# Performance work log

Hardware: AMD Instinct MI355X
Metric: run time of the kernel (lower is better)

Reference implementation:

```python
import jax, jax.numpy as jnp
import numpy as np

EPS = 1e-12  # torch F.normalize eps

def _normalize(x):
    n = jnp.linalg.norm(x, axis=-1, keepdims=True)
    return x / jnp.maximum(n, EPS)

def setup_inputs() -> dict:
    key = jax.random.key(0)
    k1, k2, k3, k4 = jax.random.split(key, 4)
    bs, P = 32, 256
    V = P * P                      # 65536 vertices
    F = 2 * (P - 1) ** 2           # 130050 faces
    C = 6                          # triangles per vertex ring
    points = jax.random.normal(k1, (bs, 3, V), dtype=jnp.float32)
    faces = jax.random.randint(k2, (F, 3), 0, V, dtype=jnp.int32)
    vert_tri_indices = jax.random.randint(k3, (V, C), 0, F, dtype=jnp.int32)
    vert_tri_weights = jax.random.uniform(k4, (V, C, 1), dtype=jnp.float32)
    return {"points": points, "faces": faces,
            "vert_tri_indices": vert_tri_indices,
            "vert_tri_weights": vert_tri_weights}

def reference(points, faces, vert_tri_indices, vert_tri_weights):
    # points: [bs, 3, V] -> vrt: [bs, V, 3]
    vrt = jnp.transpose(points, (0, 2, 1))
    # face normals: gather the 3 vertices of each face, cross, normalize
    v0 = vrt[:, faces[:, 0]]                       # [bs, F, 3]
    v1 = vrt[:, faces[:, 1]] - v0
    v2 = vrt[:, faces[:, 2]] - v0
    face_normals = _normalize(jnp.cross(v1, v2))   # [bs, F, 3]
    # vertex normals: weighted sum over each vertex's triangle ring
    fn_group = face_normals[:, vert_tri_indices]   # [bs, V, C, 3]
    vertex_normals = (fn_group * vert_tri_weights).sum(axis=-2)  # [bs, V, 3]
    return _normalize(vertex_normals)
```

## Files before the change

### kernel.cpp

```cpp
#include <hip/hip_runtime.h>
#include <hip/hip_bf16.h>


#define XCDS 8
#define BPX  4
#define FPT  2

typedef float f32x4 __attribute__((ext_vector_type(4)));

__device__ __forceinline__ float mulf_pin(float a, float b) {
  float t = a * b;
  asm("" : "+v"(t));
  return t;
}

__device__ __forceinline__ float3 cross_lhs(float ax, float ay, float az,
                                            float bx, float by, float bz) {
  float cx = __builtin_fmaf(ay, bz, -mulf_pin(az, by));
  float cy = __builtin_fmaf(az, bx, -mulf_pin(ax, bz));
  float cz = __builtin_fmaf(ax, by, -mulf_pin(ay, bx));
  return make_float3(cx, cy, cz);
}

__device__ __forceinline__ void nt_store_f4(float4* p, float x, float y,
                                            float z, float w) {
  f32x4 r;
  r[0] = x; r[1] = y; r[2] = z; r[3] = w;
  __builtin_nontemporal_store(r, (f32x4*)p);
}

__global__ __launch_bounds__(256) void rend13_pack(
    const float* __restrict__ points,
    float4*      __restrict__ ptsI,
    int V) {
  int xcd = blockIdx.x % XCDS;
  int g   = (blockIdx.x / XCDS) * 256 + threadIdx.x;
  int v   = g >> 2;
  int bl  = g & 3;
  int b   = xcd * BPX + bl;
  const float* pb = points + (size_t)b * 3 * V;
  float x = __builtin_nontemporal_load(pb + v);
  float y = __builtin_nontemporal_load(pb + V + v);
  float z = __builtin_nontemporal_load(pb + 2 * V + v);
  ptsI[((size_t)xcd * V + v) * BPX + bl] = make_float4(x, y, z, 0.0f);
}

__global__ __launch_bounds__(256) void rend13_face(
    const float4* __restrict__ ptsI,
    const int*    __restrict__ faces,
    float4*       __restrict__ fnI,
    int F, int V, int Q) {
  int xcd = blockIdx.x % XCDS;
  int g   = (blockIdx.x / XCDS) * 256 + threadIdx.x;
  int q   = g >> 2;
  int bl  = g & 3;
  if (q >= Q) return;

  int f0 = q;
  int f1 = q + Q;

  int a0 = __builtin_nontemporal_load(faces + 3 * f0 + 0);
  int a1 = __builtin_nontemporal_load(faces + 3 * f0 + 1);
  int a2 = __builtin_nontemporal_load(faces + 3 * f0 + 2);
  int b0 = __builtin_nontemporal_load(faces + 3 * f1 + 0);
  int b1 = __builtin_nontemporal_load(faces + 3 * f1 + 1);
  int b2 = __builtin_nontemporal_load(faces + 3 * f1 + 2);

  const float4* P = ptsI + (size_t)xcd * V * BPX;
  float4 pa0 = P[(size_t)a0 * BPX + bl];
  float4 pa1 = P[(size_t)a1 * BPX + bl];
  float4 pa2 = P[(size_t)a2 * BPX + bl];
  float4 pb0 = P[(size_t)b0 * BPX + bl];
  float4 pb1 = P[(size_t)b1 * BPX + bl];
  float4 pb2 = P[(size_t)b2 * BPX + bl];

  {
    float ax = pa1.x - pa0.x, ay = pa1.y - pa0.y, az = pa1.z - pa0.z;
    float bx = pa2.x - pa0.x, by = pa2.y - pa0.y, bz = pa2.z - pa0.z;
    float3 c = cross_lhs(ax, ay, az, bx, by, bz);
    float n = sqrtf((c.x * c.x + c.y * c.y) + c.z * c.z);
    float d = fmaxf(n, 1e-12f);
    nt_store_f4(fnI + ((size_t)xcd * F + f0) * BPX + bl,
                c.x / d, c.y / d, c.z / d, 0.0f);
  }
  {
    float ax = pb1.x - pb0.x, ay = pb1.y - pb0.y, az = pb1.z - pb0.z;
    float bx = pb2.x - pb0.x, by = pb2.y - pb0.y, bz = pb2.z - pb0.z;
    float3 c = cross_lhs(ax, ay, az, bx, by, bz);
    float n = sqrtf((c.x * c.x + c.y * c.y) + c.z * c.z);
    float d = fmaxf(n, 1e-12f);
    nt_store_f4(fnI + ((size_t)xcd * F + f1) * BPX + bl,
                c.x / d, c.y / d, c.z / d, 0.0f);
  }
}

__global__ __launch_bounds__(256) void rend13_vertex(
    const float4* __restrict__ fnI,
    const int*    __restrict__ vti,
    const float*  __restrict__ vtw,
    float*        __restrict__ out,
    int F, int V) {
  int xcd = blockIdx.x % XCDS;
  int g   = (blockIdx.x / XCDS) * 256 + threadIdx.x;
  int v   = g >> 2;
  int bl  = g & 3;
  if (v >= V) return;

  const int2*   t2 = (const int2*)(vti + (size_t)v * 6);
  const float2* w2 = (const float2*)(vtw + (size_t)v * 6);
  int2   t01 = t2[0], t23 = t2[1], t45 = t2[2];
  float2 w01 = w2[0], w23 = w2[1], w45 = w2[2];
  int   idx[6] = {t01.x, t01.y, t23.x, t23.y, t45.x, t45.y};
  float wgt[6] = {w01.x, w01.y, w23.x, w23.y, w45.x, w45.y};

  float sx = 0.f, sy = 0.f, sz = 0.f;
#pragma unroll
  for (int c = 0; c < 6; ++c) {
    float4 nr = fnI[((size_t)xcd * F + idx[c]) * BPX + bl];
    sx += nr.x * wgt[c];
    sy += nr.y * wgt[c];
    sz += nr.z * wgt[c];
  }

  float n = sqrtf((sx * sx + sy * sy) + sz * sz);
  float d = fmaxf(n, 1e-12f);

  int b = xcd * BPX + bl;
  size_t o = ((size_t)b * V + v) * 3;
  __builtin_nontemporal_store(sx / d, out + o + 0);
  __builtin_nontemporal_store(sy / d, out + o + 1);
  __builtin_nontemporal_store(sz / d, out + o + 2);
}

__global__ __launch_bounds__(256) void rend13_face_fb(
    const float* __restrict__ points,
    const int*   __restrict__ faces,
    float4*      __restrict__ fnorm,
    int F, int V) {
  int f = blockIdx.x * blockDim.x + threadIdx.x;
  int b = blockIdx.y;
  if (f >= F) return;

  int i0 = faces[3 * f + 0];
  int i1 = faces[3 * f + 1];
  int i2 = faces[3 * f + 2];

  const float* pb = points + (size_t)b * 3 * V;
  float ax = pb[i1] - pb[i0], ay = pb[V + i1] - pb[V + i0], az = pb[2 * V + i1] - pb[2 * V + i0];
  float bx = pb[i2] - pb[i0], by = pb[V + i2] - pb[V + i0], bz = pb[2 * V + i2] - pb[2 * V + i0];

  float3 c = cross_lhs(ax, ay, az, bx, by, bz);

  float n = sqrtf((c.x * c.x + c.y * c.y) + c.z * c.z);
  float d = fmaxf(n, 1e-12f);

  fnorm[(size_t)b * F + f] = make_float4(c.x / d, c.y / d, c.z / d, 0.0f);
}

__global__ __launch_bounds__(256) void rend13_vertex_fb(
    const float4* __restrict__ fnorm,
    const int*    __restrict__ vti,
    const float*  __restrict__ vtw,
    float*        __restrict__ out,
    int F, int V) {
  int v = blockIdx.x * blockDim.x + threadIdx.x;
  int b = blockIdx.y;
  if (v >= V) return;

  const float4* fb = fnorm + (size_t)b * F;
  float sx = 0.f, sy = 0.f, sz = 0.f;
#pragma unroll
  for (int c = 0; c < 6; ++c) {
    int    idx = vti[v * 6 + c];
    float  w   = vtw[v * 6 + c];
    float4 nr  = fb[idx];
    sx += nr.x * w;
    sy += nr.y * w;
    sz += nr.z * w;
  }
  float n = sqrtf((sx * sx + sy * sy) + sz * sz);
  float d = fmaxf(n, 1e-12f);
  size_t o = ((size_t)b * V + v) * 3;
  out[o + 0] = sx / d;
  out[o + 1] = sy / d;
  out[o + 2] = sz / d;
}

extern "C" void kernel_launch(void* const* d_in, const int* in_sizes, int n_in,
                              void* d_out, int out_size, void* d_ws, size_t ws_size,
                              hipStream_t stream) {
  const float* points = (const float*)d_in[0];
  const int*   faces  = (const int*)d_in[1];
  const int*   vti    = (const int*)d_in[2];
  const float* vtw    = (const float*)d_in[3];
  float*       out    = (float*)d_out;

  const int F  = in_sizes[1] / 3;
  const int V  = in_sizes[2] / 6;
  const int bs = (int)(in_sizes[0] / (3 * (size_t)V));

  const size_t ptsI_bytes = (size_t)bs * V * sizeof(float4);
  const size_t fnI_bytes  = (size_t)bs * F * sizeof(float4);

  const bool fast_ok = (ws_size >= ptsI_bytes + fnI_bytes) &&
                       (bs == XCDS * BPX) && (V % 256 == 0) && (F % FPT == 0);

  if (fast_ok) {
    float4* ptsI = (float4*)d_ws;
    float4* fnI  = (float4*)((char*)d_ws + ptsI_bytes);
    const int Q   = F / FPT;
    const int ppb = (V * BPX) / 256;
    const int fqb = (Q * 4 + 255) / 256;
    const int vqb = (V * BPX) / 256;

    rend13_pack<<<dim3(XCDS * ppb), dim3(256), 0, stream>>>(points, ptsI, V);
    rend13_face<<<dim3(XCDS * fqb), dim3(256), 0, stream>>>(ptsI, faces, fnI, F, V, Q);
    rend13_vertex<<<dim3(XCDS * vqb), dim3(256), 0, stream>>>(fnI, vti, vtw, out, F, V);
  } else if (ws_size >= fnI_bytes) {
    float4* fnorm = (float4*)d_ws;
    rend13_face_fb<<<dim3((F + 255) / 256, bs), dim3(256), 0, stream>>>(
        points, faces, fnorm, F, V);
    rend13_vertex_fb<<<dim3((V + 255) / 256, bs), dim3(256), 0, stream>>>(
        fnorm, vti, vtw, out, F, V);
  }
}
```

Measured before the change: 165.3 us.

## Pack intermediates as 12-byte float3 per batch lane, three faces per thread

Changes the interleaved point and face-normal workspaces from float4 per batch lane to a packed 3-float layout of 12 floats per vertex or face, which cuts intermediate memory traffic by a quarter. The face kernel now handles three faces per thread instead of two. The vertex kernel loads its indices and weights as scalar nontemporal loads. The cost is that gathers become unaligned scalar 3-float loads instead of single 16-byte vector loads, which may raise the instruction count and the number of memory transactions.

Measured after the change: 163.4 us. About the same (-1.2%).

```diff
diff --git a/kernel.cpp b/kernel.cpp
--- a/kernel.cpp
+++ b/kernel.cpp
@@ -4,9 +4,7 @@
 
 #define XCDS 8
 #define BPX  4
-#define FPT  2
-
-typedef float f32x4 __attribute__((ext_vector_type(4)));
+#define FPT  3
 
 __device__ __forceinline__ float mulf_pin(float a, float b) {
   float t = a * b;
@@ -22,16 +20,9 @@
   return make_float3(cx, cy, cz);
 }
 
-__device__ __forceinline__ void nt_store_f4(float4* p, float x, float y,
-                                            float z, float w) {
-  f32x4 r;
-  r[0] = x; r[1] = y; r[2] = z; r[3] = w;
-  __builtin_nontemporal_store(r, (f32x4*)p);
-}
-
-__global__ __launch_bounds__(256) void rend13_pack(
+__global__ __launch_bounds__(256) void rend16_pack(
     const float* __restrict__ points,
-    float4*      __restrict__ ptsI,
+    float*       __restrict__ ptsP,
     int V) {
   int xcd = blockIdx.x % XCDS;
   int g   = (blockIdx.x / XCDS) * 256 + threadIdx.x;
@@ -42,13 +33,14 @@
   float x = __builtin_nontemporal_load(pb + v);
   float y = __builtin_nontemporal_load(pb + V + v);
   float z = __builtin_nontemporal_load(pb + 2 * V + v);
-  ptsI[((size_t)xcd * V + v) * BPX + bl] = make_float4(x, y, z, 0.0f);
-}
-
-__global__ __launch_bounds__(256) void rend13_face(
-    const float4* __restrict__ ptsI,
-    const int*    __restrict__ faces,
-    float4*       __restrict__ fnI,
+  float* e = ptsP + ((size_t)xcd * V + v) * 12 + 3 * bl;
+  e[0] = x; e[1] = y; e[2] = z;
+}
+
+__global__ __launch_bounds__(256) void rend16_face(
+    const float* __restrict__ ptsP,
+    const int*   __restrict__ faces,
+    float*       __restrict__ fnP,
     int F, int V, int Q) {
   int xcd = blockIdx.x % XCDS;
   int g   = (blockIdx.x / XCDS) * 256 + threadIdx.x;
@@ -58,6 +50,7 @@
 
   int f0 = q;
   int f1 = q + Q;
+  int f2 = q + 2 * Q;
 
   int a0 = __builtin_nontemporal_load(faces + 3 * f0 + 0);
   int a1 = __builtin_nontemporal_load(faces + 3 * f0 + 1);
@@ -65,40 +58,72 @@
   int b0 = __builtin_nontemporal_load(faces + 3 * f1 + 0);
   int b1 = __builtin_nontemporal_load(faces + 3 * f1 + 1);
   int b2 = __builtin_nontemporal_load(faces + 3 * f1 + 2);
-
-  const float4* P = ptsI + (size_t)xcd * V * BPX;
-  float4 pa0 = P[(size_t)a0 * BPX + bl];
-  float4 pa1 = P[(size_t)a1 * BPX + bl];
-  float4 pa2 = P[(size_t)a2 * BPX + bl];
-  float4 pb0 = P[(size_t)b0 * BPX + bl];
-  float4 pb1 = P[(size_t)b1 * BPX + bl];
-  float4 pb2 = P[(size_t)b2 * BPX + bl];
-
+  int c0 = __builtin_nontemporal_load(faces + 3 * f2 + 0);
+  int c1 = __builtin_nontemporal_load(faces + 3 * f2 + 1);
+  int c2 = __builtin_nontemporal_load(faces + 3 * f2 + 2);
+
+  const float* P = ptsP + (size_t)xcd * V * 12 + 3 * bl;
+  const float* ea0 = P + (size_t)a0 * 12;
+  const float* ea1 = P + (size_t)a1 * 12;
+  const float* ea2 = P + (size_t)a2 * 12;
+  const float* eb0 = P + (size_t)b0 * 12;
+  const float* eb1 = P + (size_t)b1 * 12;
+  const float* eb2 = P + (size_t)b2 * 12;
+  const float* ec0 = P + (size_t)c0 * 12;
+  const float* ec1 = P + (size_t)c1 * 12;
+  const float* ec2 = P + (size_t)c2 * 12;
+
+  float a0x = ea0[0], a0y = ea0[1], a0z = ea0[2];
+  float a1x = ea1[0], a1y = ea1[1], a1z = ea1[2];
+  float a2x = ea2[0], a2y = ea2[1], a2z = ea2[2];
+  float b0x = eb0[0], b0y = eb0[1], b0z = eb0[2];
+  float b1x = eb1[0], b1y = eb1[1], b1z = eb1[2];
+  float b2x = eb2[0], b2y = eb2[1], b2z = eb2[2];
+  float c0x = ec0[0], c0y = ec0[1], c0z = ec0[2];
+  float c1x = ec1[0], c1y = ec1[1], c1z = ec1[2];
+  float c2x = ec2[0], c2y = ec2[1], c2z = ec2[2];
+
+  float* O = fnP + (size_t)xcd * F * 12 + 3 * bl;
   {
-    float ax = pa1.x - pa0.x, ay = pa1.y - pa0.y, az = pa1.z - pa0.z;
-    float bx = pa2.x - pa0.x, by = pa2.y - pa0.y, bz = pa2.z - pa0.z;
+    float ax = a1x - a0x, ay = a1y - a0y, az = a1z - a0z;
+    float bx = a2x - a0x, by = a2y - a0y, bz = a2z - a0z;
     float3 c = cross_lhs(ax, ay, az, bx, by, bz);
     float n = sqrtf((c.x * c.x + c.y * c.y) + c.z * c.z);
     float d = fmaxf(n, 1e-12f);
-    nt_store_f4(fnI + ((size_t)xcd * F + f0) * BPX + bl,
-                c.x / d, c.y / d, c.z / d, 0.0f);
+    float* o = O + (size_t)f0 * 12;
+    __builtin_nontemporal_store(c.x / d, o + 0);
+    __builtin_nontemporal_store(c.y / d, o + 1);
+    __builtin_nontemporal_store(c.z / d, o + 2);
   }
   {
-    float ax = pb1.x - pb0.x, ay = pb1.y - pb0.y, az = pb1.z - pb0.z;
-    float bx = pb2.x - pb0.x, by = pb2.y - pb0.y, bz = pb2.z - pb0.z;
+    float ax = b1x - b0x, ay = b1y - b0y, az = b1z - b0z;
+    float bx = b2x - b0x, by = b2y - b0y, bz = b2z - b0z;
     float3 c = cross_lhs(ax, ay, az, bx, by, bz);
     float n = sqrtf((c.x * c.x + c.y * c.y) + c.z * c.z);
     float d = fmaxf(n, 1e-12f);
-    nt_store_f4(fnI + ((size_t)xcd * F + f1) * BPX + bl,
-                c.x / d, c.y / d, c.z / d, 0.0f);
-  }
-}
-
-__global__ __launch_bounds__(256) void rend13_vertex(
-    const float4* __restrict__ fnI,
-    const int*    __restrict__ vti,
-    const float*  __restrict__ vtw,
-    float*        __restrict__ out,
+    float* o = O + (size_t)f1 * 12;
+    __builtin_nontemporal_store(c.x / d, o + 0);
+    __builtin_nontemporal_store(c.y / d, o + 1);
+    __builtin_nontemporal_store(c.z / d, o + 2);
+  }
+  {
+    float ax = c1x - c0x, ay = c1y - c0y, az = c1z - c0z;
+    float bx = c2x - c0x, by = c2y - c0y, bz = c2z - c0z;
+    float3 c = cross_lhs(ax, ay, az, bx, by, bz);
+    float n = sqrtf((c.x * c.x + c.y * c.y) + c.z * c.z);
+    float d = fmaxf(n, 1e-12f);
+    float* o = O + (size_t)f2 * 12;
+    __builtin_nontemporal_store(c.x / d, o + 0);
+    __builtin_nontemporal_store(c.y / d, o + 1);
+    __builtin_nontemporal_store(c.z / d, o + 2);
+  }
+}
+
+__global__ __launch_bounds__(256) void rend16_vertex(
+    const float* __restrict__ fnP,
+    const int*   __restrict__ vti,
+    const float* __restrict__ vtw,
+    float*       __restrict__ out,
     int F, int V) {
   int xcd = blockIdx.x % XCDS;
   int g   = (blockIdx.x / XCDS) * 256 + threadIdx.x;
@@ -106,21 +131,41 @@
   int bl  = g & 3;
   if (v >= V) return;
 
-  const int2*   t2 = (const int2*)(vti + (size_t)v * 6);
-  const float2* w2 = (const float2*)(vtw + (size_t)v * 6);
-  int2   t01 = t2[0], t23 = t2[1], t45 = t2[2];
-  float2 w01 = w2[0], w23 = w2[1], w45 = w2[2];
-  int   idx[6] = {t01.x, t01.y, t23.x, t23.y, t45.x, t45.y};
-  float wgt[6] = {w01.x, w01.y, w23.x, w23.y, w45.x, w45.y};
+  int i0 = __builtin_nontemporal_load(vti + (size_t)v * 6 + 0);
+  int i1 = __builtin_nontemporal_load(vti + (size_t)v * 6 + 1);
+  int i2 = __builtin_nontemporal_load(vti + (size_t)v * 6 + 2);
+  int i3 = __builtin_nontemporal_load(vti + (size_t)v * 6 + 3);
+  int i4 = __builtin_nontemporal_load(vti + (size_t)v * 6 + 4);
+  int i5 = __builtin_nontemporal_load(vti + (size_t)v * 6 + 5);
+  float w0 = __builtin_nontemporal_load(vtw + (size_t)v * 6 + 0);
+  float w1 = __builtin_nontemporal_load(vtw + (size_t)v * 6 + 1);
+  float w2 = __builtin_nontemporal_load(vtw + (size_t)v * 6 + 2);
+  float w3 = __builtin_nontemporal_load(vtw + (size_t)v * 6 + 3);
+  float w4 = __builtin_nontemporal_load(vtw + (size_t)v * 6 + 4);
+  float w5 = __builtin_nontemporal_load(vtw + (size_t)v * 6 + 5);
+
+  const float* P = fnP + (size_t)xcd * F * 12 + 3 * bl;
+  const float* e0 = P + (size_t)i0 * 12;
+  const float* e1 = P + (size_t)i1 * 12;
+  const float* e2 = P + (size_t)i2 * 12;
+  const float* e3 = P + (size_t)i3 * 12;
+  const float* e4 = P + (size_t)i4 * 12;
+  const float* e5 = P + (size_t)i5 * 12;
+
+  float n0x = e0[0], n0y = e0[1], n0z = e0[2];
+  float n1x = e1[0], n1y = e1[1], n1z = e1[2];
+  float n2x = e2[0], n2y = e2[1], n2z = e2[2];
+  float n3x = e3[0], n3y = e3[1], n3z = e3[2];
+  float n4x = e4[0], n4y = e4[1], n4z = e4[2];
+  float n5x = e5[0], n5y = e5[1], n5z = e5[2];
 
   float sx = 0.f, sy = 0.f, sz = 0.f;
-#pragma unroll
-  for (int c = 0; c < 6; ++c) {
-    float4 nr = fnI[((size_t)xcd * F + idx[c]) * BPX + bl];
-    sx += nr.x * wgt[c];
-    sy += nr.y * wgt[c];
-    sz += nr.z * wgt[c];
-  }
+  sx += n0x * w0; sy += n0y * w0; sz += n0z * w0;
+  sx += n1x * w1; sy += n1y * w1; sz += n1z * w1;
+  sx += n2x * w2; sy += n2y * w2; sz += n2z * w2;
+  sx += n3x * w3; sy += n3y * w3; sz += n3z * w3;
+  sx += n4x * w4; sy += n4y * w4; sz += n4z * w4;
+  sx += n5x * w5; sy += n5y * w5; sz += n5z * w5;
 
   float n = sqrtf((sx * sx + sy * sy) + sz * sz);
   float d = fmaxf(n, 1e-12f);
@@ -132,7 +177,7 @@
   __builtin_nontemporal_store(sz / d, out + o + 2);
 }
 
-__global__ __launch_bounds__(256) void rend13_face_fb(
+__global__ __launch_bounds__(256) void rend16_face_fb(
     const float* __restrict__ points,
     const int*   __restrict__ faces,
     float4*      __restrict__ fnorm,
@@ -157,7 +202,7 @@
   fnorm[(size_t)b * F + f] = make_float4(c.x / d, c.y / d, c.z / d, 0.0f);
 }
 
-__global__ __launch_bounds__(256) void rend13_vertex_fb(
+__global__ __launch_bounds__(256) void rend16_vertex_fb(
     const float4* __restrict__ fnorm,
     const int*    __restrict__ vti,
     const float*  __restrict__ vtw,
@@ -199,28 +244,30 @@
   const int V  = in_sizes[2] / 6;
   const int bs = (int)(in_sizes[0] / (3 * (size_t)V));
 
-  const size_t ptsI_bytes = (size_t)bs * V * sizeof(float4);
-  const size_t fnI_bytes  = (size_t)bs * F * sizeof(float4);
-
-  const bool fast_ok = (ws_size >= ptsI_bytes + fnI_bytes) &&
-                       (bs == XCDS * BPX) && (V % 256 == 0) && (F % FPT == 0);
+  const size_t ptsP_bytes = (size_t)bs * V * 12;
+  const size_t fnP_bytes  = (size_t)bs * F * 12;
+  const size_t fn_bytes   = (size_t)bs * F * sizeof(float4);
+
+  const bool fast_ok = (ws_size >= ptsP_bytes + fnP_bytes) &&
+                       (bs == XCDS * BPX) && ((V * BPX) % 256 == 0) &&
+                       (F % FPT == 0);
 
   if (fast_ok) {
-    float4* ptsI = (float4*)d_ws;
-    float4* fnI  = (float4*)((char*)d_ws + ptsI_bytes);
+    float* ptsP = (float*)d_ws;
+    float* fnP  = (float*)((char*)d_ws + ptsP_bytes);
     const int Q   = F / FPT;
     const int ppb = (V * BPX) / 256;
     const int fqb = (Q * 4 + 255) / 256;
     const int vqb = (V * BPX) / 256;
 
-    rend13_pack<<<dim3(XCDS * ppb), dim3(256), 0, stream>>>(points, ptsI, V);
-    rend13_face<<<dim3(XCDS * fqb), dim3(256), 0, stream>>>(ptsI, faces, fnI, F, V, Q);
-    rend13_vertex<<<dim3(XCDS * vqb), dim3(256), 0, stream>>>(fnI, vti, vtw, out, F, V);
-  } else if (ws_size >= fnI_bytes) {
+    rend16_pack  <<<dim3(XCDS * ppb), dim3(256), 0, stream>>>(points, ptsP, V);
+    rend16_face  <<<dim3(XCDS * fqb), dim3(256), 0, stream>>>(ptsP, faces, fnP, F, V, Q);
+    rend16_vertex<<<dim3(XCDS * vqb), dim3(256), 0, stream>>>(fnP, vti, vtw, out, F, V);
+  } else if (ws_size >= fn_bytes) {
     float4* fnorm = (float4*)d_ws;
-    rend13_face_fb<<<dim3((F + 255) / 256, bs), dim3(256), 0, stream>>>(
+    rend16_face_fb<<<dim3((F + 255) / 256, bs), dim3(256), 0, stream>>>(
         points, faces, fnorm, F, V);
-    rend13_vertex_fb<<<dim3((V + 255) / 256, bs), dim3(256), 0, stream>>>(
+    rend16_vertex_fb<<<dim3((V + 255) / 256, bs), dim3(256), 0, stream>>>(
         fnorm, vti, vtw, out, F, V);
   }
 }
```
